# Kernel optimization log

Hardware: AMD Instinct MI355X
Metric: run time of the kernel (lower is better)

## Reference

```python
import jax, jax.numpy as jnp
import numpy as np

IOU_THR = 0.5
NEG_POS = 3
CONF_W = 1.0
LOC_W = 1.0


def setup_inputs() -> dict:
    key = jax.random.key(0)
    ks = jax.random.split(key, 6)
    B, A, G = 16, 65536, 32
    ac = jax.random.uniform(ks[0], (B, A, 2))
    asz = jax.random.uniform(ks[1], (B, A, 2)) * 0.28 + 0.02
    anchors = jnp.concatenate([ac - asz / 2, ac + asz / 2], -1)
    gc = jax.random.uniform(ks[2], (B, G, 2))
    gsz = jax.random.uniform(ks[3], (B, G, 2)) * 0.28 + 0.02
    gt_boxes = jnp.concatenate([gc - gsz / 2, gc + gsz / 2], -1)
    bbox_pred = anchors + 0.05 * jax.random.normal(ks[4], (B, A, 4))
    # probabilities strictly inside (0,1) for BCE
    conf_pred = jax.random.uniform(ks[5], (B, A)) * 0.98 + 0.01
    return {"bbox_pred": bbox_pred, "conf_pred": conf_pred,
            "anchors": anchors, "gt_boxes": gt_boxes}


def _box_iou(a, g):
    # a: [A,4] xyxy, g: [G,4] xyxy -> [A,G]
    lt = jnp.maximum(a[:, None, :2], g[None, :, :2])
    rb = jnp.minimum(a[:, None, 2:], g[None, :, 2:])
    wh = jnp.clip(rb - lt, 0.0)
    inter = wh[..., 0] * wh[..., 1]
    area_a = (a[:, 2] - a[:, 0]) * (a[:, 3] - a[:, 1])
    area_g = (g[:, 2] - g[:, 0]) * (g[:, 3] - g[:, 1])
    return inter / (area_a[:, None] + area_g[None, :] - inter)


def _bce(p, t):
    return -(t * jnp.log(p) + (1.0 - t) * jnp.log1p(-p))


def _smooth_l1(x):
    ax = jnp.abs(x)
    return jnp.where(ax < 1.0, 0.5 * ax * ax, ax - 0.5)


def _per_image(bp, cp, an, gt):
    # bp: [A,4] pred boxes, cp: [A] conf, an: [A,4] anchors, gt: [G,4]
    A = cp.shape[0]
    ious = _box_iou(an, gt)                      # [A,G]
    best_gt_iou = ious.max(1)                    # [A]
    best_gt_idx = ious.argmax(1)                 # [A]
    best_anchor_idx = ious.argmax(0)             # [G] force-match each gt
    mask = (best_gt_iou > IOU_THR).at[best_anchor_idx].set(True)
    num_pos = mask.sum()

    # localization loss (center/size parameterization), summed over positives
    matched = gt[best_gt_idx]                    # [A,4]
    pc = (bp[:, :2] + bp[:, 2:]) / 2
    ps = bp[:, 2:] - bp[:, :2]
    gc = (matched[:, :2] + matched[:, 2:]) / 2
    gs = matched[:, 2:] - matched[:, :2]
    loc = _smooth_l1(jnp.concatenate([pc, ps], 1) - jnp.concatenate([gc, gs], 1)).sum(1)
    loc_loss = jnp.where(mask, loc, 0.0).sum()

    # confidence loss with hard negative mining
    t = mask.astype(cp.dtype)
    bce = _bce(cp, t)
    pos_loss = jnp.where(mask, bce, 0.0).sum()
    neg_bce = jnp.where(mask, 0.0, bce)
    num_neg = jnp.minimum(num_pos * NEG_POS, A - num_pos)
    sorted_neg = -jnp.sort(-neg_bce)             # descending
    neg_loss = jnp.where(jnp.arange(A) < num_neg, sorted_neg, 0.0).sum()
    conf_loss = pos_loss / jnp.maximum(num_pos, 1) + neg_loss / jnp.maximum(num_neg, 1)
    return loc_loss, conf_loss, num_pos


def reference(bbox_pred, conf_pred, anchors, gt_boxes):
    loc, conf, npos = jax.vmap(_per_image)(bbox_pred, conf_pred, anchors, gt_boxes)
    B = bbox_pred.shape[0]
    total_npos = jnp.maximum(npos.sum(), 1)
    total_loc = loc.sum() / total_npos * LOC_W
    total_conf = conf.sum() / B * CONF_W
    return total_loc + total_conf
```

## Files before the change

### kernel.cpp

```cpp
#include <hip/hip_runtime.h>

#define BB 16
#define AA 65536
#define GG 32
#define NB 8192
#define KOFF 59904u
#define AT 4
#define APB (256 * AT)
#define MBLK (AA / APB)
#define NSEG 64
#define SEGA (AA / NSEG)

__device__ unsigned char g_mask[(size_t)BB * AA];
__device__ unsigned char g_bidx[(size_t)BB * AA];
__device__ unsigned int  g_hpart[(size_t)BB * NSEG * (NB/2)];
__device__ float g_spart[BB * NSEG * 2];
__device__ int   g_npart[BB * NSEG];
__device__ float g_loc[BB], g_pos[BB], g_neg[BB];
__device__ int   g_npos[BB], g_nneg[BB];

#define DYN_U32 (BB * GG * 2 + 2)
__device__ unsigned int g_dyn[DYN_U32];
__device__ __forceinline__ unsigned long long* fkeyp() {
    return (unsigned long long*)g_dyn;
}
__device__ __forceinline__ int* donep() {
    return (int*)(g_dyn + BB * GG * 2);
}

__device__ __forceinline__ float midval(int bin) {
    return __uint_as_float((((unsigned int)bin + KOFF) << 14) | 8192u);
}

__global__ void __launch_bounds__(256, 4)
k_matchforce(const float4* __restrict__ anchors,
             const float4* __restrict__ gts) {
    __shared__ float4 sg[GG];
    __shared__ unsigned long long wkey[4][GG];
    const int b = blockIdx.y;
    const int t = threadIdx.x;
    const int wave = t >> 6, lane = t & 63;
    if (t < GG) sg[t] = gts[(size_t)b * GG + t];
    __syncthreads();

    const size_t abase = (size_t)b * AA + (size_t)blockIdx.x * APB;

    float ax0[AT], ay0[AT], ax1[AT], ay1[AT], aar[AT], best[AT];
    int bg[AT];
#pragma unroll
    for (int j = 0; j < AT; ++j) {
        const float4 av = anchors[abase + j * 256 + t];
        ax0[j] = av.x; ay0[j] = av.y; ax1[j] = av.z; ay1[j] = av.w;
        aar[j] = (av.z - av.x) * (av.w - av.y);
        best[j] = -1.0f; bg[j] = 0;
    }

#pragma unroll 2
    for (int g = 0; g < GG; ++g) {
        const float4 gb = sg[g];
        const float ga = (gb.z - gb.x) * (gb.w - gb.y);
        float fbest = -1.0f;
        int fo = t;
#pragma unroll
        for (int j = 0; j < AT; ++j) {
            const float lx = fmaxf(ax0[j], gb.x), ly = fmaxf(ay0[j], gb.y);
            const float rx = fminf(ax1[j], gb.z), ry = fminf(ay1[j], gb.w);
            const float w = fmaxf(rx - lx, 0.0f), h = fmaxf(ry - ly, 0.0f);
            const float inter = w * h;
            const float s = aar[j] + ga;
            const float r = inter * __builtin_amdgcn_rcpf(s);
            if (r > best[j]) { best[j] = r; bg[j] = g; }
            if (r > fbest)   { fbest = r; fo = j * 256 + t; }
        }
        unsigned long long key =
            ((unsigned long long)__float_as_uint(fbest) << 32) |
            (unsigned long long)(0xFFFFFFFFu - (unsigned int)fo);
#pragma unroll
        for (int off = 1; off < 64; off <<= 1) {
            const unsigned long long o = __shfl_xor(key, off, 64);
            if (o > key) key = o;
        }
        if (lane == 0) wkey[wave][g] = key;
    }

#pragma unroll
    for (int j = 0; j < AT; ++j) {
        g_mask[abase + j * 256 + t] = (best[j] > (1.0f / 3.0f)) ? 1 : 0;
        g_bidx[abase + j * 256 + t] = (unsigned char)bg[j];
    }
    __syncthreads();
    if (t < GG) {
        unsigned long long k = wkey[0][t];
#pragma unroll
        for (int w = 1; w < 4; ++w) {
            const unsigned long long k1 = wkey[w][t];
            if (k1 > k) k = k1;
        }
        const unsigned int off = 0xFFFFFFFFu - (unsigned int)(k & 0xFFFFFFFFull);
        const unsigned int ga = (unsigned int)(blockIdx.x * APB) + off;
        atomicMax(&fkeyp()[b * GG + t],
                  (k & 0xFFFFFFFF00000000ull) |
                  (unsigned long long)(0xFFFFFFFFu - ga));
    }
}

__global__ void k_stats(const float4* __restrict__ bbox,
                        const float* __restrict__ conf,
                        const float4* __restrict__ gts) {
    __shared__ float4 sg[GG];
    __shared__ unsigned int hp[NB / 2];
    __shared__ unsigned int bmap[SEGA / 32];
    __shared__ float rf[256], rf2[256];
    __shared__ unsigned int ru[256];
    const int b = blockIdx.y, seg = blockIdx.x, t = threadIdx.x;
    if (t < GG) sg[t] = gts[(size_t)b * GG + t];
    for (int j = t; j < NB / 2; j += 256) hp[j] = 0u;
    if (t < SEGA / 32) bmap[t] = 0u;
    __syncthreads();
    if (t < GG) {
        const unsigned long long k = fkeyp()[b * GG + t];
        const unsigned int a = 0xFFFFFFFFu - (unsigned int)(k & 0xFFFFFFFFull);
        const int la = (int)a - seg * SEGA;
        if (la >= 0 && la < SEGA) atomicOr(&bmap[la >> 5], 1u << (la & 31));
    }
    __syncthreads();

    const size_t base = (size_t)b * AA + (size_t)seg * SEGA;
    const float4* c4 = (const float4*)(conf + base);
    const uchar4* m4 = (const uchar4*)(g_mask + base);
    const uchar4* x4 = (const uchar4*)(g_bidx + base);
    const float4* bb4 = bbox + base;

    float pos = 0.0f, loc = 0.0f;
    int np = 0;
    {
        const int idx = t;
        const float4 p4 = c4[idx];
        const uchar4 mm = m4[idx];
        const uchar4 xx = x4[idx];
        const unsigned int bw = (bmap[idx >> 3] >> ((idx & 7) * 4)) & 0xFu;
        const float pv[4] = {p4.x, p4.y, p4.z, p4.w};
        const unsigned char mv[4] = {mm.x, mm.y, mm.z, mm.w};
        const unsigned char xv[4] = {xx.x, xx.y, xx.z, xx.w};
#pragma unroll
        for (int c = 0; c < 4; ++c) {
            const float p = pv[c];
            if (mv[c] | ((bw >> c) & 1u)) {
                np += 1;
                pos += -logf(p);
                const float4 bv = bb4[4 * idx + c];
                const float4 gb = sg[xv[c]];
                const float d0 = (bv.x + bv.z) * 0.5f - (gb.x + gb.z) * 0.5f;
                const float d1 = (bv.y + bv.w) * 0.5f - (gb.y + gb.w) * 0.5f;
                const float d2 = (bv.z - bv.x) - (gb.z - gb.x);
                const float d3 = (bv.w - bv.y) - (gb.w - gb.y);
                float ds[4] = {d0, d1, d2, d3};
#pragma unroll
                for (int q = 0; q < 4; ++q) {
                    float ax = fabsf(ds[q]);
                    loc += (ax < 1.0f) ? 0.5f * ax * ax : ax - 0.5f;
                }
            } else {
                const float nb = -log1pf(-p);
                int key = (int)(__float_as_uint(nb) >> 14) - (int)KOFF;
                key = key < 0 ? 0 : (key > NB - 1 ? NB - 1 : key);
                atomicAdd(&hp[key >> 1], 1u << ((key & 1) << 4));
            }
        }
    }
    ru[t] = (unsigned int)np; rf[t] = pos; rf2[t] = loc;
    __syncthreads();
    for (int w = 128; w > 0; w >>= 1) {
        if (t < w) { ru[t] += ru[t + w]; rf[t] += rf[t + w]; rf2[t] += rf2[t + w]; }
        __syncthreads();
    }
    if (t == 0) {
        g_npart[b * NSEG + seg] = (int)ru[0];
        g_spart[(b * NSEG + seg) * 2 + 0] = rf[0];
        g_spart[(b * NSEG + seg) * 2 + 1] = rf2[0];
    }
    unsigned int* outp = g_hpart + ((size_t)b * NSEG + seg) * (NB / 2);
    for (int j = t; j < NB / 2; j += 256) outp[j] = hp[j];
}

__global__ void __launch_bounds__(1024) k_select(unsigned int* __restrict__ out) {
    __shared__ unsigned int hist[NB];
    __shared__ unsigned int ru[1024];
    __shared__ unsigned int s2[32];
    __shared__ float sh_pos, sh_loc;
    __shared__ int sh_np, sh_k, sh_bsel;
    __shared__ unsigned int sh_take;
    __shared__ float rf[1024];

    const int b = blockIdx.x, t = threadIdx.x;
    for (int w = t; w < NB / 2; w += 1024) {
        unsigned int lo = 0, hi = 0;
#pragma unroll 8
        for (int s = 0; s < NSEG; ++s) {
            const unsigned int v = g_hpart[((size_t)b * NSEG + s) * (NB / 2) + w];
            lo += v & 0xFFFFu; hi += v >> 16;
        }
        hist[2 * w] = lo; hist[2 * w + 1] = hi;
    }
    if (t < 64) {
        int np = g_npart[b * NSEG + t];
        float pos = g_spart[(b * NSEG + t) * 2 + 0];
        float loc = g_spart[(b * NSEG + t) * 2 + 1];
#pragma unroll
        for (int off = 32; off > 0; off >>= 1) {
            np  += __shfl_xor(np,  off, 64);
            pos += __shfl_xor(pos, off, 64);
            loc += __shfl_xor(loc, off, 64);
        }
        if (t == 0) { sh_np = np; sh_pos = pos; sh_loc = loc; }
    }
    __syncthreads();
    const int np_tot = sh_np;

    unsigned int c = 0;
    const int hi = NB - 1 - t * 8;
#pragma unroll
    for (int j = 0; j < 8; ++j) c += hist[hi - j];
    ru[t] = c;
    __syncthreads();
    if (t < 32) {
        unsigned int x = 0;
#pragma unroll
        for (int j = 0; j < 32; ++j) x += ru[t * 32 + j];
        s2[t] = x;
    }
    __syncthreads();
    if (t == 0) {
        int k = 3 * np_tot;
        const int maxneg = AA - np_tot;
        if (k > maxneg) k = maxneg;
        sh_k = k;
        int bsel = NB;
        unsigned int take = 0;
        if (k > 0) {
            unsigned int cum = 0;
            int u = 0;
            while (u < 31 && cum + s2[u] < (unsigned int)k) { cum += s2[u]; ++u; }
            int cc = u * 32;
            while (cc < 1023 && cum + ru[cc] < (unsigned int)k) { cum += ru[cc]; ++cc; }
            const int h2 = NB - 1 - cc * 8;
            int j = 0;
            while (j < 7 && cum + hist[h2 - j] < (unsigned int)k) { cum += hist[h2 - j]; ++j; }
            bsel = h2 - j;
            take = (unsigned int)k - cum;
        }
        sh_bsel = bsel; sh_take = take;
    }
    __syncthreads();
    const int bsel = sh_bsel;
    float negp = 0.0f;
    for (int j = t; j < NB; j += 1024)
        if (j > bsel) { unsigned int cnt = hist[j]; if (cnt) negp += (float)cnt * midval(j); }
    rf[t] = negp;
    __syncthreads();
    for (int w = 512; w > 0; w >>= 1) {
        if (t < w) rf[t] += rf[t + w];
        __syncthreads();
    }
    if (t == 0) {
        float neg = 0.0f;
        if (sh_k > 0) neg = rf[0] + (float)sh_take * midval(bsel < NB ? bsel : 0);
        g_loc[b] = sh_loc; g_pos[b] = sh_pos; g_neg[b] = neg;
        g_npos[b] = np_tot; g_nneg[b] = sh_k;

        __threadfence();
        const int old = atomicAdd(donep(), 1);
        if (old == BB - 1) {
            __threadfence();
            float loc = 0.0f, conf = 0.0f;
            int tot = 0;
            for (int bb = 0; bb < BB; ++bb) {
                const float lv = __hip_atomic_load(&g_loc[bb],  __ATOMIC_RELAXED, __HIP_MEMORY_SCOPE_AGENT);
                const float pv = __hip_atomic_load(&g_pos[bb],  __ATOMIC_RELAXED, __HIP_MEMORY_SCOPE_AGENT);
                const float nv = __hip_atomic_load(&g_neg[bb],  __ATOMIC_RELAXED, __HIP_MEMORY_SCOPE_AGENT);
                const int   np = __hip_atomic_load(&g_npos[bb], __ATOMIC_RELAXED, __HIP_MEMORY_SCOPE_AGENT);
                const int   nn = __hip_atomic_load(&g_nneg[bb], __ATOMIC_RELAXED, __HIP_MEMORY_SCOPE_AGENT);
                loc += lv;
                conf += pv / (float)(np > 1 ? np : 1) +
                        nv / (float)(nn > 1 ? nn : 1);
                tot += np;
            }
            const float total = loc / (float)(tot > 1 ? tot : 1) + conf / (float)BB;
            const unsigned int u = __float_as_uint(total);
            const unsigned int r = 0x7FFFu + ((u >> 16) & 1u);
            const unsigned int bf = (u + r) >> 16;
            out[0] = (bf << 16) | bf;
        }
    }
}

extern "C" void kernel_launch(void* const* d_in, const int* in_sizes, int n_in,
                              void* d_out, int out_size, void* d_ws, size_t ws_size,
                              hipStream_t stream) {
    const float4* bbox    = (const float4*)d_in[0];
    const float*  conf    = (const float*)d_in[1];
    const float4* anchors = (const float4*)d_in[2];
    const float4* gts     = (const float4*)d_in[3];

    static unsigned int* dynp = nullptr;
    if (!dynp) hipGetSymbolAddress((void**)&dynp, HIP_SYMBOL(g_dyn));
    hipMemsetAsync(dynp, 0, sizeof(unsigned int) * DYN_U32, stream);

    k_matchforce<<<dim3(MBLK, BB), 256, 0, stream>>>(anchors, gts);
    k_stats<<<dim3(NSEG, BB), 256, 0, stream>>>(bbox, conf, gts);
    k_select<<<BB, 1024, 0, stream>>>((unsigned int*)d_out);
}
```

Before: 141.7 us.

## Emit compact negative key lists instead of per-segment histograms

Each k_stats block used to build and write a full 8192-bin packed histogram to global memory, and k_select summed 64 such histograms per image. Now each block writes only its negative-sample keys (16-bit) compactly, and k_select builds the histogram with shared-memory atomics from those lists. This cuts global traffic roughly from 16KB per segment to about 2KB, at the cost of more LDS atomics in the single select block per image. AT is also raised from 4 to 8 for the match kernel.

```diff
diff --git a/kernel.cpp b/kernel.cpp
--- a/kernel.cpp
+++ b/kernel.cpp
@@ -5,15 +5,16 @@
 #define GG 32
 #define NB 8192
 #define KOFF 59904u
-#define AT 4
+#define AT 8
 #define APB (256 * AT)
 #define MBLK (AA / APB)
 #define NSEG 64
 #define SEGA (AA / NSEG)
 
-__device__ unsigned char g_mask[(size_t)BB * AA];
-__device__ unsigned char g_bidx[(size_t)BB * AA];
-__device__ unsigned int  g_hpart[(size_t)BB * NSEG * (NB/2)];
+__device__ unsigned char  g_mask[(size_t)BB * AA];
+__device__ unsigned char  g_bidx[(size_t)BB * AA];
+__device__ unsigned short g_nkey[(size_t)BB * NSEG * SEGA];
+__device__ int   g_ncnt[BB * NSEG];
 __device__ float g_spart[BB * NSEG * 2];
 __device__ int   g_npart[BB * NSEG];
 __device__ float g_loc[BB], g_pos[BB], g_neg[BB];
@@ -108,14 +109,15 @@
                         const float* __restrict__ conf,
                         const float4* __restrict__ gts) {
     __shared__ float4 sg[GG];
-    __shared__ unsigned int hp[NB / 2];
     __shared__ unsigned int bmap[SEGA / 32];
+    __shared__ unsigned short nk[SEGA];
+    __shared__ unsigned int ncnt;
     __shared__ float rf[256], rf2[256];
     __shared__ unsigned int ru[256];
     const int b = blockIdx.y, seg = blockIdx.x, t = threadIdx.x;
     if (t < GG) sg[t] = gts[(size_t)b * GG + t];
-    for (int j = t; j < NB / 2; j += 256) hp[j] = 0u;
     if (t < SEGA / 32) bmap[t] = 0u;
+    if (t == 0) ncnt = 0u;
     __syncthreads();
     if (t < GG) {
         const unsigned long long k = fkeyp()[b * GG + t];
@@ -142,6 +144,8 @@
         const float pv[4] = {p4.x, p4.y, p4.z, p4.w};
         const unsigned char mv[4] = {mm.x, mm.y, mm.z, mm.w};
         const unsigned char xv[4] = {xx.x, xx.y, xx.z, xx.w};
+        unsigned short lk[4];
+        int ln = 0;
 #pragma unroll
         for (int c = 0; c < 4; ++c) {
             const float p = pv[c];
@@ -164,12 +168,17 @@
                 const float nb = -log1pf(-p);
                 int key = (int)(__float_as_uint(nb) >> 14) - (int)KOFF;
                 key = key < 0 ? 0 : (key > NB - 1 ? NB - 1 : key);
-                atomicAdd(&hp[key >> 1], 1u << ((key & 1) << 4));
+                lk[ln++] = (unsigned short)key;
             }
         }
+        if (ln) {
+            const unsigned int slot = atomicAdd(&ncnt, (unsigned int)ln);
+            for (int i = 0; i < ln; ++i) nk[slot + i] = lk[i];
+        }
     }
     ru[t] = (unsigned int)np; rf[t] = pos; rf2[t] = loc;
     __syncthreads();
+    if (t == 0 && (ncnt & 1u)) nk[ncnt] = 0xFFFFu;
     for (int w = 128; w > 0; w >>= 1) {
         if (t < w) { ru[t] += ru[t + w]; rf[t] += rf[t + w]; rf2[t] += rf2[t + w]; }
         __syncthreads();
@@ -178,30 +187,27 @@
         g_npart[b * NSEG + seg] = (int)ru[0];
         g_spart[(b * NSEG + seg) * 2 + 0] = rf[0];
         g_spart[(b * NSEG + seg) * 2 + 1] = rf2[0];
-    }
-    unsigned int* outp = g_hpart + ((size_t)b * NSEG + seg) * (NB / 2);
-    for (int j = t; j < NB / 2; j += 256) outp[j] = hp[j];
+        g_ncnt[b * NSEG + seg] = (int)ncnt;
+    }
+    const unsigned int cw = (ncnt + 1u) >> 1;
+    const unsigned int* nk32 = (const unsigned int*)nk;
+    unsigned int* outk = (unsigned int*)(g_nkey + ((size_t)b * NSEG + seg) * SEGA);
+    for (unsigned int j = t; j < cw; j += 256) outk[j] = nk32[j];
 }
 
 __global__ void __launch_bounds__(1024) k_select(unsigned int* __restrict__ out) {
     __shared__ unsigned int hist[NB];
     __shared__ unsigned int ru[1024];
     __shared__ unsigned int s2[32];
+    __shared__ int scnt[NSEG];
     __shared__ float sh_pos, sh_loc;
     __shared__ int sh_np, sh_k, sh_bsel;
     __shared__ unsigned int sh_take;
     __shared__ float rf[1024];
 
     const int b = blockIdx.x, t = threadIdx.x;
-    for (int w = t; w < NB / 2; w += 1024) {
-        unsigned int lo = 0, hi = 0;
-#pragma unroll 8
-        for (int s = 0; s < NSEG; ++s) {
-            const unsigned int v = g_hpart[((size_t)b * NSEG + s) * (NB / 2) + w];
-            lo += v & 0xFFFFu; hi += v >> 16;
-        }
-        hist[2 * w] = lo; hist[2 * w + 1] = hi;
-    }
+    for (int j = t; j < NB; j += 1024) hist[j] = 0u;
+    if (t < NSEG) scnt[t] = g_ncnt[b * NSEG + t];
     if (t < 64) {
         int np = g_npart[b * NSEG + t];
         float pos = g_spart[(b * NSEG + t) * 2 + 0];
@@ -213,6 +219,19 @@
             loc += __shfl_xor(loc, off, 64);
         }
         if (t == 0) { sh_np = np; sh_pos = pos; sh_loc = loc; }
+    }
+    __syncthreads();
+    for (int s = 0; s < NSEG; ++s) {
+        const unsigned int cnt = (unsigned int)scnt[s];
+        const unsigned int cw = (cnt + 1u) >> 1;
+        const unsigned int* kp =
+            (const unsigned int*)(g_nkey + ((size_t)b * NSEG + s) * SEGA);
+        for (unsigned int j = t; j < cw; j += 1024) {
+            const unsigned int v = kp[j];
+            atomicAdd(&hist[v & 0xFFFFu], 1u);
+            const unsigned int k1 = v >> 16;
+            if (k1 != 0xFFFFu) atomicAdd(&hist[k1], 1u);
+        }
     }
     __syncthreads();
     const int np_tot = sh_np;
```

Measured after the change: 155.8 us. 1.1x slower.
